# Performance work log

Measured on AMD Instinct MI355X. Metric: run time of the kernel, lower is better.

The kernel has to match this reference:

```python
import jax, jax.numpy as jnp
import numpy as np

N = 50000   # nodes
E = 800000  # edges (avg degree 16)
C = 128     # hidden_channels
G = 128     # graphs in batch
L0, L1 = 512, 256  # linear_hidden_channels
P = 2       # num_params (output per graph)


def setup_inputs() -> dict:
    key = jax.random.key(0)
    ks = iter(jax.random.split(key, 48))

    def w(shape):
        return jax.random.normal(next(ks), shape, jnp.float32) / np.float32(np.sqrt(shape[0]))

    inp = {}
    inp["x"] = jax.random.normal(next(ks), (N, 4), jnp.float32)
    inp["edge_index"] = jax.random.randint(next(ks), (2, E), 0, N, dtype=jnp.int32)
    inp["edge_attr"] = jax.random.normal(next(ks), (E, 3), jnp.float32)
    inp["batch"] = jnp.sort(jax.random.randint(next(ks), (N,), 0, G, dtype=jnp.int32))
    # TransformerConv params: layer 0 (in=4) and shared layer (in=C, applied twice
    # because `[GConv(...)]*(n-1)` reuses the same module object).
    for i, din in enumerate([4, C]):
        inp[f"Wq{i}"] = w((din, C)); inp[f"bq{i}"] = jnp.zeros((C,), jnp.float32)
        inp[f"Wk{i}"] = w((din, C)); inp[f"bk{i}"] = jnp.zeros((C,), jnp.float32)
        inp[f"Wv{i}"] = w((din, C)); inp[f"bv{i}"] = jnp.zeros((C,), jnp.float32)
        inp[f"We{i}"] = w((3, C))   # lin_edge has no bias
        inp[f"Ws{i}"] = w((din, C)); inp[f"bs{i}"] = jnp.zeros((C,), jnp.float32)
    inp["Wl0"] = w((C, L0));  inp["bl0"] = jnp.zeros((L0,), jnp.float32)
    inp["Wl1"] = w((L0, L1)); inp["bl1"] = jnp.zeros((L1,), jnp.float32)
    inp["Wl2"] = w((L1, P));  inp["bl2"] = jnp.zeros((P,), jnp.float32)
    return inp


def tconv(x, src, dst, e_attr, Wq, bq, Wk, bk, Wv, bv, We, Ws, bs):
    # TransformerConv (heads=1, edge_dim, root_weight=True, beta=False)
    n = x.shape[0]
    c = Wq.shape[1]
    q = x @ Wq + bq            # [N, C]
    k = x @ Wk + bk
    v = x @ Wv + bv
    e = e_attr @ We            # [E, C]
    kj = k[src] + e            # [E, C] key at source + edge emb
    vj = v[src] + e            # [E, C] value at source + edge emb
    logits = jnp.sum(q[dst] * kj, axis=-1) / jnp.sqrt(jnp.float32(c))  # [E]
    # softmax over incoming edges of each target node
    m = jax.ops.segment_max(logits, dst, num_segments=n)
    a = jnp.exp(logits - m[dst])
    denom = jax.ops.segment_sum(a, dst, num_segments=n)
    alpha = a / denom[dst]
    out = jax.ops.segment_sum(vj * alpha[:, None], dst, num_segments=n)
    return out + x @ Ws + bs   # root/skip connection


def reference(x, edge_index, edge_attr, batch,
              Wq0, bq0, Wk0, bk0, Wv0, bv0, We0, Ws0, bs0,
              Wq1, bq1, Wk1, bk1, Wv1, bv1, We1, Ws1, bs1,
              Wl0, bl0, Wl1, bl1, Wl2, bl2):
    src, dst = edge_index[0], edge_index[1]
    # layer 0
    h = tconv(x, src, dst, edge_attr, Wq0, bq0, Wk0, bk0, Wv0, bv0, We0, Ws0, bs0)
    h = jax.nn.leaky_relu(h, 0.01)  # dropout is identity in eval
    # layers 1..2 share weights (Python list-multiplication of modules)
    for _ in range(2):
        h = tconv(h, src, dst, edge_attr, Wq1, bq1, Wk1, bk1, Wv1, bv1, We1, Ws1, bs1)
        h = jax.nn.leaky_relu(h, 0.01)
    # global_add_pool
    g = jax.ops.segment_sum(h, batch, num_segments=G)  # [G, C]
    # MLP head
    g = jax.nn.relu(g @ Wl0 + bl0)
    g = jax.nn.relu(g @ Wl1 + bl1)
    g = g @ Wl2 + bl2                                  # [G, 2]
    return jnp.ravel(g)                                # [G*2]
```

## Files before the change

### kernel.cpp

```cpp
#include <hip/hip_runtime.h>
#include <math.h>

#define N_NODES 50000
#define N_EDGES 800000
#define CDIM    128
#define GDIM    128
#define L0DIM   512
#define L1DIM   256

typedef unsigned int uint;
typedef unsigned short ushort;
typedef __attribute__((ext_vector_type(8))) short short8;
typedef __attribute__((ext_vector_type(4))) float f32x4;

__device__ inline ushort f2bf(float f) {
  uint u = __float_as_uint(f);
  uint r = (u + 0x7fffu + ((u >> 16) & 1u)) >> 16;
  return (ushort)r;
}
__device__ inline float bflo(uint u) { return __uint_as_float(u << 16); }
__device__ inline float bfhi(uint u) { return __uint_as_float(u & 0xffff0000u); }

__global__ void hist_kernel(const int* __restrict__ dst, int* counts, int E) {
  int e = blockIdx.x * 256 + threadIdx.x;
  if (e < E) atomicAdd(&counts[dst[e]], 1);
}

__global__ void scan_blocks(const int* __restrict__ counts, int* excl, int* bsums, int N) {
  __shared__ int s[1024];
  int tid = threadIdx.x;
  int i = blockIdx.x * 1024 + tid;
  int v = (i < N) ? counts[i] : 0;
  s[tid] = v;
  __syncthreads();
  for (int off = 1; off < 1024; off <<= 1) {
    int t = (tid >= off) ? s[tid - off] : 0;
    __syncthreads();
    s[tid] += t;
    __syncthreads();
  }
  if (i < N) excl[i] = s[tid] - v;
  if (tid == 1023) bsums[blockIdx.x] = s[1023];
}

__global__ void scan_sums(int* bsums, int nb) {
  if (threadIdx.x == 0) {
    int run = 0;
    for (int b = 0; b < nb; b++) { int t = bsums[b]; bsums[b] = run; run += t; }
  }
}

__global__ void scan_add(const int* __restrict__ excl, const int* __restrict__ bsums,
                         int* indptr, int N, int E) {
  int i = blockIdx.x * 1024 + threadIdx.x;
  if (i < N) indptr[i] = excl[i] + bsums[blockIdx.x];
  if (i == 0) indptr[N] = E;
}

__global__ void scatter2_kernel(const int* __restrict__ dst, const int* __restrict__ src,
                                const float* __restrict__ attr,
                                const int* __restrict__ indptr,
                                int* cursor, int* csr_src, float4* csr_attr, int E) {
  int e = blockIdx.x * 256 + threadIdx.x;
  if (e < E) {
    int d = dst[e];
    int pos = atomicAdd(&cursor[d], 1);
    int i = indptr[d] + pos;
    csr_src[i] = src[e];
    csr_attr[i] = make_float4(attr[e * 3 + 0], attr[e * 3 + 1], attr[e * 3 + 2], 0.f);
  }
}

__global__ void l0_qkvs(const float* __restrict__ x,
                        const float* __restrict__ Wq, const float* __restrict__ bq,
                        const float* __restrict__ Wk, const float* __restrict__ bk,
                        const float* __restrict__ Wv, const float* __restrict__ bv,
                        const float* __restrict__ Ws, const float* __restrict__ bs,
                        float* __restrict__ q, ushort* __restrict__ kvb,
                        float* __restrict__ hs, int N) {
  __shared__ float W[4][4][128];
  __shared__ float B[4][128];
  int tid = threadIdx.x;
  for (int i = tid; i < 4 * 128; i += 256) {
    W[0][i >> 7][i & 127] = Wq[i];
    W[1][i >> 7][i & 127] = Wk[i];
    W[2][i >> 7][i & 127] = Wv[i];
    W[3][i >> 7][i & 127] = Ws[i];
  }
  for (int i = tid; i < 128; i += 256) {
    B[0][i] = bq[i]; B[1][i] = bk[i]; B[2][i] = bv[i]; B[3][i] = bs[i];
  }
  __syncthreads();
  int gid = blockIdx.x * 256 + tid;
  int n = gid >> 7, c = gid & 127;
  if (n >= N) return;
  float x0 = x[n * 4 + 0], x1 = x[n * 4 + 1], x2 = x[n * 4 + 2], x3 = x[n * 4 + 3];
  float qv = x0 * W[0][0][c] + x1 * W[0][1][c] + x2 * W[0][2][c] + x3 * W[0][3][c] + B[0][c];
  float kv = x0 * W[1][0][c] + x1 * W[1][1][c] + x2 * W[1][2][c] + x3 * W[1][3][c] + B[1][c];
  float vv = x0 * W[2][0][c] + x1 * W[2][1][c] + x2 * W[2][2][c] + x3 * W[2][3][c] + B[2][c];
  float sv = x0 * W[3][0][c] + x1 * W[3][1][c] + x2 * W[3][2][c] + x3 * W[3][3][c] + B[3][c];
  q[n * 128 + c] = qv;
  kvb[(size_t)n * 256 + c]       = f2bf(kv);
  kvb[(size_t)n * 256 + 128 + c] = f2bf(vv);
  hs[n * 128 + c] = sv;
}

__global__ void prep_w(const float* __restrict__ Wq, const float* __restrict__ Wk,
                       const float* __restrict__ Wv, const float* __restrict__ Ws,
                       ushort* __restrict__ wt) {
  int idx = blockIdx.x * 256 + threadIdx.x;
  int z = idx >> 14, rem = idx & 16383;
  int k_ = rem >> 7, c_ = rem & 127;
  const float* W = (z == 0) ? Wq : (z == 1) ? Wk : (z == 2) ? Wv : Ws;
  wt[z * 16384 + c_ * 128 + k_] = f2bf(W[k_ * 128 + c_]);
}

#define LDA 136
__global__ __launch_bounds__(256) void gemm_mfma(
    const float* __restrict__ H, const ushort* __restrict__ wtg,
    const float* __restrict__ bq, const float* __restrict__ bk,
    const float* __restrict__ bv, const float* __restrict__ bs,
    float* __restrict__ q, ushort* __restrict__ kvb,
    float* __restrict__ hs, int N) {
  int z = blockIdx.z;
  const float* bb = (z == 0) ? bq : (z == 1) ? bk : (z == 2) ? bv : bs;
  __shared__ ushort Alds[64 * LDA];
  __shared__ ushort Wlds[128 * LDA];
  int tid = threadIdx.x;
  int n0 = blockIdx.x * 64;

  {
    const uint* wg = (const uint*)(wtg + z * 16384);
    uint* wl = (uint*)Wlds;
    for (int i = tid; i < 8192; i += 256) {
      int c_ = i >> 6, kp = i & 63;
      wl[c_ * (LDA / 2) + kp] = wg[c_ * 64 + kp];
    }
  }
  {
    uint* al = (uint*)Alds;
    for (int i = tid; i < 4096; i += 256) {
      int r = i >> 6, kp = i & 63;
      int grow = n0 + r; grow = (grow < N) ? grow : (N - 1);
      float2 hv = *(const float2*)&H[(size_t)grow * 128 + 2 * kp];
      al[r * (LDA / 2) + kp] = (uint)f2bf(hv.x) | ((uint)f2bf(hv.y) << 16);
    }
  }
  __syncthreads();

  int w = tid >> 6, lane = tid & 63;
  int m_ = lane & 15, quad = lane >> 4;
  f32x4 acc[8];
#pragma unroll
  for (int ct = 0; ct < 8; ct++) acc[ct] = 0.f;

#pragma unroll
  for (int kc = 0; kc < 4; kc++) {
    short8 af = *(const short8*)&Alds[(w * 16 + m_) * LDA + kc * 32 + quad * 8];
#pragma unroll
    for (int ct = 0; ct < 8; ct++) {
      short8 bf = *(const short8*)&Wlds[(ct * 16 + m_) * LDA + kc * 32 + quad * 8];
      acc[ct] = __builtin_amdgcn_mfma_f32_16x16x32_bf16(af, bf, acc[ct], 0, 0, 0);
    }
  }

#pragma unroll
  for (int ct = 0; ct < 8; ct++) {
    int col = ct * 16 + m_;
    float bcol = bb[col];
#pragma unroll
    for (int reg = 0; reg < 4; reg++) {
      int n = n0 + w * 16 + quad * 4 + reg;
      if (n < N) {
        float o = acc[ct][reg] + bcol;
        if (z == 0)      q[(size_t)n * 128 + col] = o;
        else if (z == 3) hs[(size_t)n * 128 + col] = o;
        else             kvb[(size_t)n * 256 + ((z == 2) ? 128 : 0) + col] = f2bf(o);
      }
    }
  }
}

__global__ __launch_bounds__(256) void attn_fused(
    const float* __restrict__ q, const ushort* __restrict__ kv,
    const int* __restrict__ indptr, const int* __restrict__ csr_src,
    const float4* __restrict__ csr_attr, const float* __restrict__ We,
    float* __restrict__ h, int N) {
  __shared__ float WeS[384];
  int tid = threadIdx.x;
  for (int i = tid; i < 384; i += 256) WeS[i] = We[i];
  __syncthreads();
  int lane = tid & 63;
  int n = blockIdx.x * 4 + (tid >> 6);
  if (n >= N) return;
  int g = lane >> 4, gl = lane & 15;
  int c = gl * 8;
  float w0[8], w1[8], w2[8];
#pragma unroll
  for (int j = 0; j < 8; j++) {
    w0[j] = WeS[c + j]; w1[j] = WeS[128 + c + j]; w2[j] = WeS[256 + c + j];
  }
  float4 qa = *(const float4*)&q[(size_t)n * 128 + c];
  float4 qb4 = *(const float4*)&q[(size_t)n * 128 + c + 4];
  float qv[8] = {qa.x, qa.y, qa.z, qa.w, qb4.x, qb4.y, qb4.z, qb4.w};
  float4 sk0 = *(const float4*)&h[(size_t)n * 128 + c];
  float4 sk1 = *(const float4*)&h[(size_t)n * 128 + c + 4];
  int beg = indptr[n], end = indptr[n + 1];

  if (end > beg) {
    float m = -3.4e38f, d = 0.f;
    float acc[8];
#pragma unroll
    for (int j = 0; j < 8; j++) acc[j] = 0.f;
    const uint* kvw = (const uint*)kv;
    int i = beg + g;
    int sj = 0; float4 at = make_float4(0.f, 0.f, 0.f, 0.f);
    if (i < end) { sj = csr_src[i]; at = csr_attr[i]; }
    for (; i < end; i += 4) {
      int sjc = sj; float4 atc = at;
      int inx = i + 4;
      if (inx < end) { sj = csr_src[inx]; at = csr_attr[inx]; }
      const uint4* kp = (const uint4*)(kvw + (size_t)sjc * 128);
      uint4 kr = kp[gl];
      uint4 vr = kp[16 + gl];
      float kx[8], vx[8];
      kx[0] = bflo(kr.x); kx[1] = bfhi(kr.x); kx[2] = bflo(kr.y); kx[3] = bfhi(kr.y);
      kx[4] = bflo(kr.z); kx[5] = bfhi(kr.z); kx[6] = bflo(kr.w); kx[7] = bfhi(kr.w);
      vx[0] = bflo(vr.x); vx[1] = bfhi(vr.x); vx[2] = bflo(vr.y); vx[3] = bfhi(vr.y);
      vx[4] = bflo(vr.z); vx[5] = bfhi(vr.z); vx[6] = bflo(vr.w); vx[7] = bfhi(vr.w);
      float p = 0.f;
      float u_[8];
#pragma unroll
      for (int j = 0; j < 8; j++) {
        float ee = atc.x * w0[j] + atc.y * w1[j] + atc.z * w2[j];
        p = fmaf(qv[j], kx[j] + ee, p);
        u_[j] = vx[j] + ee;
      }
      p += __shfl_xor(p, 1); p += __shfl_xor(p, 2);
      p += __shfl_xor(p, 4); p += __shfl_xor(p, 8);
      float l = p * 0.08838834764831845f;
      float nm = fmaxf(m, l);
      float sf = __expf(m - nm);
      float a = __expf(l - nm);
      d = d * sf + a;
#pragma unroll
      for (int j = 0; j < 8; j++) acc[j] = acc[j] * sf + a * u_[j];
      m = nm;
    }
#pragma unroll
    for (int off = 16; off < 64; off <<= 1) {
      float m2 = __shfl_xor(m, off);
      float d2 = __shfl_xor(d, off);
      float nm = fmaxf(m, m2);
      float s1 = __expf(m - nm), s2 = __expf(m2 - nm);
      d = d * s1 + d2 * s2;
#pragma unroll
      for (int j = 0; j < 8; j++) {
        float a2 = __shfl_xor(acc[j], off);
        acc[j] = acc[j] * s1 + a2 * s2;
      }
      m = nm;
    }
    float inv = 1.f / d;
    sk0.x += acc[0] * inv; sk0.y += acc[1] * inv;
    sk0.z += acc[2] * inv; sk0.w += acc[3] * inv;
    sk1.x += acc[4] * inv; sk1.y += acc[5] * inv;
    sk1.z += acc[6] * inv; sk1.w += acc[7] * inv;
  }
  sk0.x = (sk0.x > 0.f) ? sk0.x : 0.01f * sk0.x;
  sk0.y = (sk0.y > 0.f) ? sk0.y : 0.01f * sk0.y;
  sk0.z = (sk0.z > 0.f) ? sk0.z : 0.01f * sk0.z;
  sk0.w = (sk0.w > 0.f) ? sk0.w : 0.01f * sk0.w;
  sk1.x = (sk1.x > 0.f) ? sk1.x : 0.01f * sk1.x;
  sk1.y = (sk1.y > 0.f) ? sk1.y : 0.01f * sk1.y;
  sk1.z = (sk1.z > 0.f) ? sk1.z : 0.01f * sk1.z;
  sk1.w = (sk1.w > 0.f) ? sk1.w : 0.01f * sk1.w;
  if (g == 0) {
    *(float4*)&h[(size_t)n * 128 + c] = sk0;
    *(float4*)&h[(size_t)n * 128 + c + 4] = sk1;
  }
}

__global__ void pool_kernel(const float* __restrict__ h, const int* __restrict__ batch,
                            float* __restrict__ gout, int N) {
  int c = threadIdx.x;
  int n0 = blockIdx.x * 128;
  if (n0 >= N) return;
  int n1 = min(n0 + 128, N);
  float acc = 0.f;
  int cur = batch[n0];
  for (int n = n0; n < n1; n++) {
    int b = batch[n];
    if (b != cur) { atomicAdd(&gout[cur * 128 + c], acc); acc = 0.f; cur = b; }
    acc += h[(size_t)n * 128 + c];
  }
  atomicAdd(&gout[cur * 128 + c], acc);
}

__global__ __launch_bounds__(256) void mlp_fused(
    const float* __restrict__ gp,
    const float* __restrict__ Wl0, const float* __restrict__ bl0,
    const float* __restrict__ Wl1, const float* __restrict__ bl1,
    const float* __restrict__ Wl2, const float* __restrict__ bl2,
    float* __restrict__ out) {
  int g = blockIdx.x;
  int tid = threadIdx.x;
  __shared__ float xin[CDIM];
  __shared__ float h1[L0DIM];
  __shared__ float h2[L1DIM];
  __shared__ float r0s[4], r1s[4];
  if (tid < CDIM) xin[tid] = gp[g * CDIM + tid];
  __syncthreads();
  for (int c = tid; c < L0DIM; c += 256) {
    float a0 = 0.f, a1 = 0.f, a2 = 0.f, a3 = 0.f;
#pragma unroll 4
    for (int kk = 0; kk < CDIM; kk += 4) {
      a0 = fmaf(xin[kk + 0], Wl0[(kk + 0) * L0DIM + c], a0);
      a1 = fmaf(xin[kk + 1], Wl0[(kk + 1) * L0DIM + c], a1);
      a2 = fmaf(xin[kk + 2], Wl0[(kk + 2) * L0DIM + c], a2);
      a3 = fmaf(xin[kk + 3], Wl0[(kk + 3) * L0DIM + c], a3);
    }
    h1[c] = fmaxf((a0 + a1) + (a2 + a3) + bl0[c], 0.f);
  }
  __syncthreads();
  {
    int c = tid;
    float a0 = 0.f, a1 = 0.f, a2 = 0.f, a3 = 0.f;
#pragma unroll 4
    for (int kk = 0; kk < L0DIM; kk += 4) {
      a0 = fmaf(h1[kk + 0], Wl1[(kk + 0) * L1DIM + c], a0);
      a1 = fmaf(h1[kk + 1], Wl1[(kk + 1) * L1DIM + c], a1);
      a2 = fmaf(h1[kk + 2], Wl1[(kk + 2) * L1DIM + c], a2);
      a3 = fmaf(h1[kk + 3], Wl1[(kk + 3) * L1DIM + c], a3);
    }
    h2[c] = fmaxf((a0 + a1) + (a2 + a3) + bl1[c], 0.f);
  }
  __syncthreads();
  float p0 = h2[tid] * Wl2[tid * 2 + 0];
  float p1 = h2[tid] * Wl2[tid * 2 + 1];
#pragma unroll
  for (int off = 32; off > 0; off >>= 1) {
    p0 += __shfl_down(p0, off);
    p1 += __shfl_down(p1, off);
  }
  int wv = tid >> 6, ln = tid & 63;
  if (ln == 0) { r0s[wv] = p0; r1s[wv] = p1; }
  __syncthreads();
  if (tid == 0) out[g * 2 + 0] = r0s[0] + r0s[1] + r0s[2] + r0s[3] + bl2[0];
  if (tid == 1) out[g * 2 + 1] = r1s[0] + r1s[1] + r1s[2] + r1s[3] + bl2[1];
}

extern "C" void kernel_launch(void* const* d_in, const int* in_sizes, int n_in,
                              void* d_out, int out_size, void* d_ws, size_t ws_size,
                              hipStream_t stream) {
  const int N = N_NODES, E = N_EDGES;
  const float* x    = (const float*)d_in[0];
  const int*   ei   = (const int*)d_in[1];
  const float* attr = (const float*)d_in[2];
  const int*   batch= (const int*)d_in[3];
  const int* src = ei;
  const int* dst = ei + E;

  const float *Wq0 = (const float*)d_in[4],  *bq0 = (const float*)d_in[5];
  const float *Wk0 = (const float*)d_in[6],  *bk0 = (const float*)d_in[7];
  const float *Wv0 = (const float*)d_in[8],  *bv0 = (const float*)d_in[9];
  const float *We0 = (const float*)d_in[10];
  const float *Ws0 = (const float*)d_in[11], *bs0 = (const float*)d_in[12];
  const float *Wq1 = (const float*)d_in[13], *bq1 = (const float*)d_in[14];
  const float *Wk1 = (const float*)d_in[15], *bk1 = (const float*)d_in[16];
  const float *Wv1 = (const float*)d_in[17], *bv1 = (const float*)d_in[18];
  const float *We1 = (const float*)d_in[19];
  const float *Ws1 = (const float*)d_in[20], *bs1 = (const float*)d_in[21];
  const float *Wl0 = (const float*)d_in[22], *bl0 = (const float*)d_in[23];
  const float *Wl1 = (const float*)d_in[24], *bl1 = (const float*)d_in[25];
  const float *Wl2 = (const float*)d_in[26], *bl2 = (const float*)d_in[27];

  size_t off = 0;
  auto carve = [&](size_t bytes) {
    void* p = (char*)d_ws + off;
    off += (bytes + 255) & ~(size_t)255;
    return p;
  };
  float*  hA       = (float*)carve((size_t)N * CDIM * 4);
  float*  hB       = (float*)carve((size_t)N * CDIM * 4);
  float*  qb       = (float*)carve((size_t)N * CDIM * 4);
  ushort* kvb      = (ushort*)carve((size_t)N * 256 * 2);
  int*    indptr   = (int*)carve((size_t)(N + 1) * 4);
  int*    csr_src  = (int*)carve((size_t)E * 4);
  float4* csr_attr = (float4*)carve((size_t)E * 16);
  int*    counts   = (int*)carve((size_t)N * 4);
  int*    cursor   = (int*)carve((size_t)N * 4);
  int*    excl     = (int*)carve((size_t)N * 4);
  int*    bsums    = (int*)carve((size_t)64 * 4);
  ushort* wt1      = (ushort*)carve((size_t)4 * 16384 * 2);
  float*  gp       = (float*)carve((size_t)GDIM * CDIM * 4);

  hipMemsetAsync(counts, 0, (size_t)N * 4, stream);
  hipMemsetAsync(cursor, 0, (size_t)N * 4, stream);
  hipMemsetAsync(gp, 0, (size_t)GDIM * CDIM * 4, stream);

  int nscan = (N + 1023) / 1024;
  hist_kernel<<<(E + 255) / 256, 256, 0, stream>>>(dst, counts, E);
  scan_blocks<<<nscan, 1024, 0, stream>>>(counts, excl, bsums, N);
  scan_sums<<<1, 64, 0, stream>>>(bsums, nscan);
  scan_add<<<nscan, 1024, 0, stream>>>(excl, bsums, indptr, N, E);
  scatter2_kernel<<<(E + 255) / 256, 256, 0, stream>>>(dst, src, attr, indptr, cursor,
                                                       csr_src, csr_attr, E);
  prep_w<<<256, 256, 0, stream>>>(Wq1, Wk1, Wv1, Ws1, wt1);

  int naBlocks = (N + 3) / 4;
  dim3 gemmGrid((N + 63) / 64, 1, 4);

  l0_qkvs<<<(N * 128 + 255) / 256, 256, 0, stream>>>(
      x, Wq0, bq0, Wk0, bk0, Wv0, bv0, Ws0, bs0, qb, kvb, hA, N);
  attn_fused<<<naBlocks, 256, 0, stream>>>(qb, kvb, indptr, csr_src, csr_attr, We0, hA, N);

  gemm_mfma<<<gemmGrid, 256, 0, stream>>>(hA, wt1, bq1, bk1, bv1, bs1, qb, kvb, hB, N);
  attn_fused<<<naBlocks, 256, 0, stream>>>(qb, kvb, indptr, csr_src, csr_attr, We1, hB, N);

  gemm_mfma<<<gemmGrid, 256, 0, stream>>>(hB, wt1, bq1, bk1, bv1, bs1, qb, kvb, hA, N);
  attn_fused<<<naBlocks, 256, 0, stream>>>(qb, kvb, indptr, csr_src, csr_attr, We1, hA, N);

  pool_kernel<<<(N + 127) / 128, 128, 0, stream>>>(hA, batch, gp, N);
  mlp_fused<<<GDIM, 256, 0, stream>>>(gp, Wl0, bl0, Wl1, bl1, Wl2, bl2, (float*)d_out);
}
```

Before: 640.1 us.

## Factor edge embedding out of attention loop, parallelize bsum scan and pooling

```diff
diff --git a/kernel.cpp b/kernel.cpp
--- a/kernel.cpp
+++ b/kernel.cpp
@@ -44,10 +44,15 @@
 }
 
 __global__ void scan_sums(int* bsums, int nb) {
-  if (threadIdx.x == 0) {
-    int run = 0;
-    for (int b = 0; b < nb; b++) { int t = bsums[b]; bsums[b] = run; run += t; }
-  }
+  int lane = threadIdx.x;
+  int orig = (lane < nb) ? bsums[lane] : 0;
+  int v = orig;
+#pragma unroll
+  for (int off = 1; off < 64; off <<= 1) {
+    int t = __shfl_up(v, off);
+    if (lane >= off) v += t;
+  }
+  if (lane < nb) bsums[lane] = v - orig;
 }
 
 __global__ void scan_add(const int* __restrict__ excl, const int* __restrict__ bsums,
@@ -195,20 +200,35 @@
   if (n >= N) return;
   int g = lane >> 4, gl = lane & 15;
   int c = gl * 8;
-  float w0[8], w1[8], w2[8];
-#pragma unroll
-  for (int j = 0; j < 8; j++) {
-    w0[j] = WeS[c + j]; w1[j] = WeS[128 + c + j]; w2[j] = WeS[256 + c + j];
-  }
-  float4 qa = *(const float4*)&q[(size_t)n * 128 + c];
+  float4 qa  = *(const float4*)&q[(size_t)n * 128 + c];
   float4 qb4 = *(const float4*)&q[(size_t)n * 128 + c + 4];
   float qv[8] = {qa.x, qa.y, qa.z, qa.w, qb4.x, qb4.y, qb4.z, qb4.w};
+  float we0[8], we1[8], we2[8];
+#pragma unroll
+  for (int j = 0; j < 8; j++) {
+    we0[j] = WeS[c + j]; we1[j] = WeS[128 + c + j]; we2[j] = WeS[256 + c + j];
+  }
+  float t0 = 0.f, t1 = 0.f, t2 = 0.f;
+#pragma unroll
+  for (int j = 0; j < 8; j++) {
+    t0 = fmaf(we0[j], qv[j], t0);
+    t1 = fmaf(we1[j], qv[j], t1);
+    t2 = fmaf(we2[j], qv[j], t2);
+  }
+#pragma unroll
+  for (int off = 1; off < 16; off <<= 1) {
+    t0 += __shfl_xor(t0, off);
+    t1 += __shfl_xor(t1, off);
+    t2 += __shfl_xor(t2, off);
+  }
+
   float4 sk0 = *(const float4*)&h[(size_t)n * 128 + c];
   float4 sk1 = *(const float4*)&h[(size_t)n * 128 + c + 4];
   int beg = indptr[n], end = indptr[n + 1];
 
   if (end > beg) {
     float m = -3.4e38f, d = 0.f;
+    float sa0 = 0.f, sa1 = 0.f, sa2 = 0.f;
     float acc[8];
 #pragma unroll
     for (int j = 0; j < 8; j++) acc[j] = 0.f;
@@ -229,22 +249,23 @@
       vx[0] = bflo(vr.x); vx[1] = bfhi(vr.x); vx[2] = bflo(vr.y); vx[3] = bfhi(vr.y);
       vx[4] = bflo(vr.z); vx[5] = bfhi(vr.z); vx[6] = bflo(vr.w); vx[7] = bfhi(vr.w);
       float p = 0.f;
-      float u_[8];
-#pragma unroll
-      for (int j = 0; j < 8; j++) {
-        float ee = atc.x * w0[j] + atc.y * w1[j] + atc.z * w2[j];
-        p = fmaf(qv[j], kx[j] + ee, p);
-        u_[j] = vx[j] + ee;
-      }
+#pragma unroll
+      for (int j = 0; j < 8; j++) p = fmaf(qv[j], kx[j], p);
       p += __shfl_xor(p, 1); p += __shfl_xor(p, 2);
       p += __shfl_xor(p, 4); p += __shfl_xor(p, 8);
+      p = fmaf(atc.x, t0, p);
+      p = fmaf(atc.y, t1, p);
+      p = fmaf(atc.z, t2, p);
       float l = p * 0.08838834764831845f;
       float nm = fmaxf(m, l);
       float sf = __expf(m - nm);
       float a = __expf(l - nm);
       d = d * sf + a;
-#pragma unroll
-      for (int j = 0; j < 8; j++) acc[j] = acc[j] * sf + a * u_[j];
+      sa0 = sa0 * sf + a * atc.x;
+      sa1 = sa1 * sf + a * atc.y;
+      sa2 = sa2 * sf + a * atc.z;
+#pragma unroll
+      for (int j = 0; j < 8; j++) acc[j] = fmaf(acc[j], sf, a * vx[j]);
       m = nm;
     }
 #pragma unroll
@@ -254,6 +275,9 @@
       float nm = fmaxf(m, m2);
       float s1 = __expf(m - nm), s2 = __expf(m2 - nm);
       d = d * s1 + d2 * s2;
+      sa0 = sa0 * s1 + __shfl_xor(sa0, off) * s2;
+      sa1 = sa1 * s1 + __shfl_xor(sa1, off) * s2;
+      sa2 = sa2 * s1 + __shfl_xor(sa2, off) * s2;
 #pragma unroll
       for (int j = 0; j < 8; j++) {
         float a2 = __shfl_xor(acc[j], off);
@@ -262,10 +286,14 @@
       m = nm;
     }
     float inv = 1.f / d;
-    sk0.x += acc[0] * inv; sk0.y += acc[1] * inv;
-    sk0.z += acc[2] * inv; sk0.w += acc[3] * inv;
-    sk1.x += acc[4] * inv; sk1.y += acc[5] * inv;
-    sk1.z += acc[6] * inv; sk1.w += acc[7] * inv;
+    float o[8];
+#pragma unroll
+    for (int j = 0; j < 8; j++) {
+      float ecorr = sa0 * we0[j] + sa1 * we1[j] + sa2 * we2[j];
+      o[j] = (acc[j] + ecorr) * inv;
+    }
+    sk0.x += o[0]; sk0.y += o[1]; sk0.z += o[2]; sk0.w += o[3];
+    sk1.x += o[4]; sk1.y += o[5]; sk1.z += o[6]; sk1.w += o[7];
   }
   sk0.x = (sk0.x > 0.f) ? sk0.x : 0.01f * sk0.x;
   sk0.y = (sk0.y > 0.f) ? sk0.y : 0.01f * sk0.y;
@@ -283,18 +311,26 @@
 
 __global__ void pool_kernel(const float* __restrict__ h, const int* __restrict__ batch,
                             float* __restrict__ gout, int N) {
-  int c = threadIdx.x;
-  int n0 = blockIdx.x * 128;
+  int tid = threadIdx.x;
+  int sub = tid >> 6;
+  int c = 2 * (tid & 63);
+  int n0 = blockIdx.x * 64 + sub * 16;
   if (n0 >= N) return;
-  int n1 = min(n0 + 128, N);
-  float acc = 0.f;
+  int n1 = min(n0 + 16, N);
+  float a0 = 0.f, a1 = 0.f;
   int cur = batch[n0];
   for (int n = n0; n < n1; n++) {
     int b = batch[n];
-    if (b != cur) { atomicAdd(&gout[cur * 128 + c], acc); acc = 0.f; cur = b; }
-    acc += h[(size_t)n * 128 + c];
-  }
-  atomicAdd(&gout[cur * 128 + c], acc);
+    if (b != cur) {
+      atomicAdd(&gout[cur * 128 + c], a0);
+      atomicAdd(&gout[cur * 128 + c + 1], a1);
+      a0 = 0.f; a1 = 0.f; cur = b;
+    }
+    float2 hv = *(const float2*)&h[(size_t)n * 128 + c];
+    a0 += hv.x; a1 += hv.y;
+  }
+  atomicAdd(&gout[cur * 128 + c], a0);
+  atomicAdd(&gout[cur * 128 + c + 1], a1);
 }
 
 __global__ __launch_bounds__(256) void mlp_fused(
@@ -388,15 +424,15 @@
   int*    indptr   = (int*)carve((size_t)(N + 1) * 4);
   int*    csr_src  = (int*)carve((size_t)E * 4);
   float4* csr_attr = (float4*)carve((size_t)E * 16);
-  int*    counts   = (int*)carve((size_t)N * 4);
-  int*    cursor   = (int*)carve((size_t)N * 4);
+  int*    cc       = (int*)carve((size_t)2 * N * 4);
+  int*    counts   = cc;
+  int*    cursor   = cc + N;
   int*    excl     = (int*)carve((size_t)N * 4);
   int*    bsums    = (int*)carve((size_t)64 * 4);
   ushort* wt1      = (ushort*)carve((size_t)4 * 16384 * 2);
   float*  gp       = (float*)carve((size_t)GDIM * CDIM * 4);
 
-  hipMemsetAsync(counts, 0, (size_t)N * 4, stream);
-  hipMemsetAsync(cursor, 0, (size_t)N * 4, stream);
+  hipMemsetAsync(cc, 0, (size_t)2 * N * 4, stream);
   hipMemsetAsync(gp, 0, (size_t)GDIM * CDIM * 4, stream);
 
   int nscan = (N + 1023) / 1024;
@@ -421,6 +457,6 @@
   gemm_mfma<<<gemmGrid, 256, 0, stream>>>(hB, wt1, bq1, bk1, bv1, bs1, qb, kvb, hA, N);
   attn_fused<<<naBlocks, 256, 0, stream>>>(qb, kvb, indptr, csr_src, csr_attr, We1, hA, N);
 
-  pool_kernel<<<(N + 127) / 128, 128, 0, stream>>>(hA, batch, gp, N);
+  pool_kernel<<<(N + 63) / 64, 256, 0, stream>>>(hA, batch, gp, N);
   mlp_fused<<<GDIM, 256, 0, stream>>>(gp, Wl0, bl0, Wl1, bl1, Wl2, bl2, (float*)d_out);
 }
```

After: 586.6 us. 8.4% less time.
